# Performance work log

Hardware: AMD Instinct MI355X
Metric: run time of the kernel (lower is better)

## Reference

```python
import jax, jax.numpy as jnp
import numpy as np
from math import factorial

LMAX = 2
C_DIM = 128
N = 50000
# (l1, l2, l_out) 'uuu' (channel-wise, no weights) instructions, as in the module ([:3])
INSTR = [(2, 2, 0), (1, 2, 1), (1, 1, 2)]


def _f(n):
    return float(factorial(int(n)))


def _su2_cg(j1, m1, j2, m2, j3, m3):
    # Clebsch-Gordan <j1 m1 j2 m2 | j3 m3> (Racah formula), complex SU(2) basis
    if m3 != m1 + m2:
        return 0.0
    vmin = int(max(-j1 + j2 + m3, -j1 + m1, 0))
    vmax = int(min(j2 + j3 + m1, j3 - j1 + j2, j3 + m3))
    pref = ((2 * j3 + 1) * _f(j3 + j1 - j2) * _f(j3 - j1 + j2) * _f(j1 + j2 - j3) / _f(j1 + j2 + j3 + 1)
            * _f(j3 + m3) * _f(j3 - m3) / (_f(j1 - m1) * _f(j1 + m1) * _f(j2 - m2) * _f(j2 + m2))) ** 0.5
    s = 0.0
    for v in range(vmin, vmax + 1):
        s += (-1.0) ** (v + j2 + m2) / _f(v) * _f(j2 + j3 + m1 - v) * _f(j1 - m1 + v) / (
            _f(j3 - j1 + j2 - v) * _f(j3 + m3 - v) * _f(v + j1 - j2 - m3))
    return pref * s


def _q_real_to_complex(l):
    # e3nn change-of-basis from real to complex spherical harmonics
    q = np.zeros((2 * l + 1, 2 * l + 1), dtype=np.complex128)
    for m in range(-l, 0):
        q[l + m, l + abs(m)] = 1.0 / np.sqrt(2)
        q[l + m, l - abs(m)] = -1j / np.sqrt(2)
    q[l, l] = 1.0
    for m in range(1, l + 1):
        q[l + m, l + abs(m)] = (-1) ** m / np.sqrt(2)
        q[l + m, l - abs(m)] = 1j * (-1) ** m / np.sqrt(2)
    return (-1j) ** l * q


def wigner_3j(l1, l2, l3):
    # real-basis Wigner 3j, unit Frobenius norm (e3nn convention)
    Csu2 = np.zeros((2 * l1 + 1, 2 * l2 + 1, 2 * l3 + 1), dtype=np.complex128)
    for i, m1 in enumerate(range(-l1, l1 + 1)):
        for k, m2 in enumerate(range(-l2, l2 + 1)):
            for n, m3 in enumerate(range(-l3, l3 + 1)):
                Csu2[i, k, n] = _su2_cg(l1, m1, l2, m2, l3, m3)
    Q1, Q2, Q3 = _q_real_to_complex(l1), _q_real_to_complex(l2), _q_real_to_complex(l3)
    C = np.einsum('ij,kl,mn,ikn->jlm', Q1, Q2, np.conj(Q3.T), Csu2)
    assert np.abs(C.imag).max() < 1e-7
    C = C.real
    return (C / np.linalg.norm(C)).astype(np.float32)


W3J = {(l1, l2, lo): jnp.asarray(wigner_3j(l1, l2, lo)) for (l1, l2, lo) in INSTR}


def so3_linear(x, W, b):
    # per-degree block-diagonal linear; x: [N, (LMAX+1)^2, Cin], W: [LMAX+1, Cout, Cin], b: [Cout] (l=0 only)
    outs = []
    for l in range(LMAX + 1):
        y = jnp.einsum('nmc,dc->nmd', x[:, l * l:(l + 1) * (l + 1), :], W[l])
        if l == 0:
            y = y + b
        outs.append(y)
    return jnp.concatenate(outs, axis=1)


def tensor_product_uuu(x1, x2):
    # sparse CG tensor product, channel-shared ('uuu'), no path weights
    out = jnp.zeros_like(x1)
    for (l1, l2, lo) in INSTR:
        w3j = W3J[(l1, l2, lo)]
        alpha = float((2 * lo + 1) ** 0.5)  # component normalization
        blk = alpha * jnp.einsum('ijk,nic,njc->nkc', w3j,
                                 x1[:, l1 * l1:(l1 + 1) ** 2, :],
                                 x2[:, l2 * l2:(l2 + 1) ** 2, :])
        out = out.at[:, lo * lo:(lo + 1) ** 2, :].add(blk)
    return out


def setup_inputs() -> dict:
    key = jax.random.key(0)
    ks = jax.random.split(key, 7)
    scale = 1.0 / np.sqrt(C_DIM)
    m_dim = (LMAX + 1) ** 2  # 9
    return {
        'irreps_x': jax.random.normal(ks[0], (N, m_dim, C_DIM), jnp.float32),
        'W_left': jax.random.normal(ks[1], (LMAX + 1, C_DIM, C_DIM), jnp.float32) * scale,
        'b_left': jax.random.normal(ks[2], (C_DIM,), jnp.float32) * scale,
        'W_right': jax.random.normal(ks[3], (LMAX + 1, C_DIM, C_DIM), jnp.float32) * scale,
        'b_right': jax.random.normal(ks[4], (C_DIM,), jnp.float32) * scale,
        'W_final': jax.random.normal(ks[5], (LMAX + 1, C_DIM, C_DIM), jnp.float32) * scale,
        'b_final': jax.random.normal(ks[6], (C_DIM,), jnp.float32) * scale,
    }


def reference(irreps_x, W_left, b_left, W_right, b_right, W_final, b_final):
    xl = so3_linear(irreps_x, W_left, b_left)
    xr = so3_linear(irreps_x, W_right, b_right)
    out = tensor_product_uuu(xl, xr)
    return so3_linear(out, W_final, b_final)  # [N, 9, C]
```

## Files before the change

### kernel.cpp

```cpp
#include <hip/hip_runtime.h>
#include <cmath>
#include <complex>

typedef unsigned short u16;
typedef __bf16 bf16x8 __attribute__((ext_vector_type(8)));
typedef float f32x4 __attribute__((ext_vector_type(4)));

#define CD 128
#define TILE_N 8
#define XS 136
#define LS 128

#define SMEM_TOTAL (72 * XS + 64 * LS + 64 * LS)

struct TPW { float w220[25]; float w121[45]; float w112[45]; };

__device__ __forceinline__ u16 f2b(float f) {
  unsigned u = __float_as_uint(f);
  u += 0x7fffu + ((u >> 16) & 1u);
  return (u16)(u >> 16);
}
__device__ __forceinline__ float b2f(u16 h) {
  return __uint_as_float(((unsigned)h) << 16);
}

__global__ void cvt_weights_kernel(const float* __restrict__ Wl,
                                   const float* __restrict__ Wr,
                                   const float* __restrict__ Wf,
                                   u16* __restrict__ ws) {
  int idx = blockIdx.x * 256 + threadIdx.x;
  const float* src; int off;
  if (idx < 49152)      { src = Wl; off = idx; }
  else if (idx < 98304) { src = Wr; off = idx - 49152; }
  else                  { src = Wf; off = idx - 98304; }
  ws[idx] = f2b(src[off]);
}

__global__ __launch_bounds__(256, 3)
void fused_kernel(const float* __restrict__ x, const u16* __restrict__ ws,
                  const float* __restrict__ bfin, float* __restrict__ out,
                  int N, TPW tw) {
  __shared__ __align__(16) u16 smem[SMEM_TOTAL];
  u16* bufX = smem;
  u16* sTP  = smem;
  u16* sL   = smem + 72 * XS;
  u16* sR   = smem + 72 * XS + 64 * LS;

  const int tid  = threadIdx.x;
  const int n0   = blockIdx.x * TILE_N;
  const int w    = tid >> 6;
  const int lane = tid & 63;
  const int q    = lane >> 4;
  const int lr   = lane & 15;

#pragma unroll
  for (int it = 0; it < 4; ++it) {
    int e = (it * 256 + tid) * 8;
    int r = e >> 7;
    int c = e & 127;
    int n = n0 + (r & 7);
    if (n >= N) n = N - 1;
    int grow = (n * 9 + 1 + (r >> 3)) * CD + c;
    float4 a = *(const float4*)(x + grow);
    float4 b = *(const float4*)(x + grow + 4);
    uint4 v;
    v.x = (unsigned)f2b(a.x) | ((unsigned)f2b(a.y) << 16);
    v.y = (unsigned)f2b(a.z) | ((unsigned)f2b(a.w) << 16);
    v.z = (unsigned)f2b(b.x) | ((unsigned)f2b(b.y) << 16);
    v.w = (unsigned)f2b(b.z) | ((unsigned)f2b(b.w) << 16);
    *(uint4*)(bufX + r * XS + c) = v;
  }
  __syncthreads();

#pragma unroll
  for (int cti = 0; cti < 4; ++cti) {
    int ct   = w * 4 + cti;
    int mat  = ct >> 3;
    int dcol = ((ct & 7) << 4) + lr;
    const u16* w1 = ws + (mat * 3 + 1) * 16384 + dcol * CD;
    const u16* w2 = ws + (mat * 3 + 2) * 16384 + dcol * CD;
    uint4 b1[4], b2[4];
#pragma unroll
    for (int kk = 0; kk < 4; ++kk) {
      b1[kk] = *(const uint4*)(w1 + kk * 32 + q * 8);
      b2[kk] = *(const uint4*)(w2 + kk * 32 + q * 8);
    }
    u16* dst = (ct < 8) ? sL : sR;
#pragma unroll
    for (int rt = 0; rt < 5; ++rt) {
      const int l2f   = (rt >= 2) ? 1 : 0;
      const int rows  = l2f ? 40 : 24;
      const int gbase = l2f ? (rt - 2) * 16 : rt * 16;
      const int boff  = l2f ? 24 : 0;
      int ga = gbase + lr; if (ga > rows - 1) ga = rows - 1;
      const int arow = boff + ga;
      f32x4 acc = {0.f, 0.f, 0.f, 0.f};
#pragma unroll
      for (int kk = 0; kk < 4; ++kk) {
        uint4 av = *(const uint4*)(bufX + arow * XS + kk * 32 + q * 8);
        acc = __builtin_amdgcn_mfma_f32_16x16x32_bf16(
            __builtin_bit_cast(bf16x8, av),
            __builtin_bit_cast(bf16x8, l2f ? b2[kk] : b1[kk]),
            acc, 0, 0, 0);
      }
#pragma unroll
      for (int reg = 0; reg < 4; ++reg) {
        int gg = gbase + q * 4 + reg;
        if (gg < rows) dst[(boff + gg) * LS + dcol] = f2b(acc[reg]);
      }
    }
  }
  __syncthreads();

  {
    int c  = tid & 127;
    int nb = tid >> 7;
#pragma unroll
    for (int p = 0; p < 4; ++p) {
      int n = nb * 4 + p;
      float xl1[3], xr1[3], xl2[5], xr2[5];
#pragma unroll
      for (int i = 0; i < 3; ++i) {
        xl1[i] = b2f(sL[(i * 8 + n) * LS + c]);
        xr1[i] = b2f(sR[(i * 8 + n) * LS + c]);
      }
#pragma unroll
      for (int j = 0; j < 5; ++j) {
        xl2[j] = b2f(sL[(24 + j * 8 + n) * LS + c]);
        xr2[j] = b2f(sR[(24 + j * 8 + n) * LS + c]);
      }
      float o0 = 0.f;
#pragma unroll
      for (int i = 0; i < 5; ++i)
#pragma unroll
        for (int j = 0; j < 5; ++j)
          o0 += tw.w220[i * 5 + j] * xl2[i] * xr2[j];
      float o1[3] = {0.f, 0.f, 0.f};
#pragma unroll
      for (int i = 0; i < 3; ++i)
#pragma unroll
        for (int j = 0; j < 5; ++j) {
          float pr = xl1[i] * xr2[j];
#pragma unroll
          for (int k = 0; k < 3; ++k) o1[k] += tw.w121[(i * 5 + j) * 3 + k] * pr;
        }
      float o2[5] = {0.f, 0.f, 0.f, 0.f, 0.f};
#pragma unroll
      for (int i = 0; i < 3; ++i)
#pragma unroll
        for (int j = 0; j < 3; ++j) {
          float pr = xl1[i] * xr1[j];
#pragma unroll
          for (int k = 0; k < 5; ++k) o2[k] += tw.w112[(i * 3 + j) * 5 + k] * pr;
        }
      sTP[(0 * 8 + n) * XS + c] = f2b(o0);
#pragma unroll
      for (int k = 0; k < 3; ++k) sTP[((1 + k) * 8 + n) * XS + c] = f2b(o1[k]);
#pragma unroll
      for (int k = 0; k < 5; ++k) sTP[((4 + k) * 8 + n) * XS + c] = f2b(o2[k]);
    }
  }
  __syncthreads();

#pragma unroll
  for (int cti = 0; cti < 2; ++cti) {
    int ct   = w + cti * 4;
    int dcol = (ct << 4) + lr;
    float bias = bfin[dcol];
    const u16* wfb = ws + 6 * 16384 + dcol * CD;
#pragma unroll
    for (int l = 0; l < 3; ++l) {
      const u16* wf = wfb + l * 16384;
      uint4 bfrag[4];
#pragma unroll
      for (int kk = 0; kk < 4; ++kk)
        bfrag[kk] = *(const uint4*)(wf + kk * 32 + q * 8);
      const int rows   = (l == 0) ? 8 : (l == 1 ? 24 : 40);
      const int soff   = (l == 0) ? 0 : (l == 1 ? 8 : 32);
      const int ntiles = (l == 0) ? 1 : (l == 1 ? 2 : 3);
      for (int t = 0; t < ntiles; ++t) {
        int ga = t * 16 + lr; if (ga > rows - 1) ga = rows - 1;
        const int arow = soff + ga;
        f32x4 acc = {0.f, 0.f, 0.f, 0.f};
#pragma unroll
        for (int kk = 0; kk < 4; ++kk) {
          uint4 av = *(const uint4*)(sTP + arow * XS + kk * 32 + q * 8);
          acc = __builtin_amdgcn_mfma_f32_16x16x32_bf16(
              __builtin_bit_cast(bf16x8, av),
              __builtin_bit_cast(bf16x8, bfrag[kk]),
              acc, 0, 0, 0);
        }
#pragma unroll
        for (int reg = 0; reg < 4; ++reg) {
          int gg = t * 16 + q * 4 + reg;
          if (gg < rows) {
            int m = l * l + (gg >> 3);
            int n = n0 + (gg & 7);
            if (n < N) {
              float v = acc[reg];
              if (l == 0) v += bias;
              out[(n * 9 + m) * CD + dcol] = v;
            }
          }
        }
      }
    }
  }
}

typedef std::complex<double> cd;

static double factd(int n) { double r = 1.0; for (int i = 2; i <= n; ++i) r *= i; return r; }

static double su2_cg(int j1, int m1, int j2, int m2, int j3, int m3) {
  if (m3 != m1 + m2) return 0.0;
  int vmin = -j1 + j2 + m3; if (-j1 + m1 > vmin) vmin = -j1 + m1; if (0 > vmin) vmin = 0;
  int vmax = j2 + j3 + m1; if (j3 - j1 + j2 < vmax) vmax = j3 - j1 + j2; if (j3 + m3 < vmax) vmax = j3 + m3;
  double pref = std::sqrt((2.0 * j3 + 1.0) * factd(j3 + j1 - j2) * factd(j3 - j1 + j2)
                          * factd(j1 + j2 - j3) / factd(j1 + j2 + j3 + 1)
                          * factd(j3 + m3) * factd(j3 - m3)
                          / (factd(j1 - m1) * factd(j1 + m1) * factd(j2 - m2) * factd(j2 + m2)));
  double s = 0.0;
  for (int v = vmin; v <= vmax; ++v) {
    double sgn = ((v + j2 + m2) & 1) ? -1.0 : 1.0;
    s += sgn / factd(v) * factd(j2 + j3 + m1 - v) * factd(j1 - m1 + v)
         / (factd(j3 - j1 + j2 - v) * factd(j3 + m3 - v) * factd(v + j1 - j2 - m3));
  }
  return pref * s;
}

static void qmat(int l, cd q[5][5]) {
  for (int a = 0; a < 5; ++a) for (int b = 0; b < 5; ++b) q[a][b] = 0.0;
  const double is2 = 1.0 / std::sqrt(2.0);
  for (int m = -l; m < 0; ++m) {
    q[l + m][l - m] = is2;
    q[l + m][l + m] = cd(0.0, -is2);
  }
  q[l][l] = 1.0;
  for (int m = 1; m <= l; ++m) {
    double s = (m & 1) ? -1.0 : 1.0;
    q[l + m][l + m] = s * is2;
    q[l + m][l - m] = cd(0.0, s * is2);
  }
  cd f(1.0, 0.0);
  for (int i = 0; i < l; ++i) f *= cd(0.0, -1.0);
  for (int a = 0; a < 5; ++a) for (int b = 0; b < 5; ++b) q[a][b] *= f;
}

static void wigner3j(int l1, int l2, int l3, double* C) {
  int d1 = 2 * l1 + 1, d2 = 2 * l2 + 1, d3 = 2 * l3 + 1;
  cd Q1[5][5], Q2[5][5], Q3[5][5];
  qmat(l1, Q1); qmat(l2, Q2); qmat(l3, Q3);
  cd Csu2[5][5][5];
  for (int i = 0; i < d1; ++i)
    for (int k = 0; k < d2; ++k)
      for (int n = 0; n < d3; ++n)
        Csu2[i][k][n] = su2_cg(l1, i - l1, l2, k - l2, l3, n - l3);
  double norm = 0.0;
  for (int j = 0; j < d1; ++j)
    for (int lx = 0; lx < d2; ++lx)
      for (int m = 0; m < d3; ++m) {
        cd acc(0.0, 0.0);
        for (int i = 0; i < d1; ++i)
          for (int k = 0; k < d2; ++k)
            for (int n = 0; n < d3; ++n)
              acc += Q1[i][j] * Q2[k][lx] * std::conj(Q3[n][m]) * Csu2[i][k][n];
        C[(j * d2 + lx) * d3 + m] = acc.real();
        norm += acc.real() * acc.real();
      }
  norm = std::sqrt(norm);
  for (int t = 0; t < d1 * d2 * d3; ++t) C[t] /= norm;
}

extern "C" void kernel_launch(void* const* d_in, const int* in_sizes, int n_in,
                              void* d_out, int out_size, void* d_ws, size_t ws_size,
                              hipStream_t stream) {
  const float* x    = (const float*)d_in[0];
  const float* Wl   = (const float*)d_in[1];
  const float* Wr   = (const float*)d_in[3];
  const float* Wf   = (const float*)d_in[5];
  const float* bfin = (const float*)d_in[6];
  float* out = (float*)d_out;
  const int N = in_sizes[0] / (9 * CD);

  TPW tw;
  double c220[25], c121[45], c112[45];
  wigner3j(2, 2, 0, c220);
  wigner3j(1, 2, 1, c121);
  wigner3j(1, 1, 2, c112);
  const double a1 = std::sqrt(3.0), a2 = std::sqrt(5.0);
  for (int i = 0; i < 25; ++i) tw.w220[i] = (float)c220[i];
  for (int i = 0; i < 45; ++i) tw.w121[i] = (float)(a1 * c121[i]);
  for (int i = 0; i < 45; ++i) tw.w112[i] = (float)(a2 * c112[i]);

  u16* ws = (u16*)d_ws;
  cvt_weights_kernel<<<576, 256, 0, stream>>>(Wl, Wr, Wf, ws);
  int grid = (N + TILE_N - 1) / TILE_N;
  fused_kernel<<<grid, 256, 0, stream>>>(x, ws, bfin, out, N, tw);
}
```

Baseline: 522.5 us.

## Restructure fused kernel: prefetch weight fragments, reuse A tiles, vectorize TP stage

Weight B-fragments for the left/right linears and the bias are loaded before the x tile is staged, so their global latency overlaps the input conversion. Each wave now owns one matrix and reuses loaded A fragments across two column tiles. The final linear computes two column tiles per A load and prefetches its weights before the barrier. The tensor-product stage handles two channels per thread with 32-bit LDS accesses, and the LDS row stride is padded to 132. The weight-conversion kernel is vectorized to 8 elements per thread. Holding more fragments in flight raises register pressure, which may hurt occupancy under the launch bounds of 3 blocks.

```diff
diff --git a/kernel.cpp b/kernel.cpp
--- a/kernel.cpp
+++ b/kernel.cpp
@@ -3,13 +3,14 @@
 #include <complex>
 
 typedef unsigned short u16;
+typedef unsigned int u32;
 typedef __bf16 bf16x8 __attribute__((ext_vector_type(8)));
 typedef float f32x4 __attribute__((ext_vector_type(4)));
 
 #define CD 128
 #define TILE_N 8
 #define XS 136
-#define LS 128
+#define LS 132
 
 #define SMEM_TOTAL (72 * XS + 64 * LS + 64 * LS)
 
@@ -23,17 +24,27 @@
 __device__ __forceinline__ float b2f(u16 h) {
   return __uint_as_float(((unsigned)h) << 16);
 }
+__device__ __forceinline__ u32 pack2(float a, float b) {
+  return (u32)f2b(a) | ((u32)f2b(b) << 16);
+}
 
 __global__ void cvt_weights_kernel(const float* __restrict__ Wl,
                                    const float* __restrict__ Wr,
                                    const float* __restrict__ Wf,
                                    u16* __restrict__ ws) {
-  int idx = blockIdx.x * 256 + threadIdx.x;
+  int idx = (blockIdx.x * 256 + threadIdx.x) * 8;
   const float* src; int off;
   if (idx < 49152)      { src = Wl; off = idx; }
   else if (idx < 98304) { src = Wr; off = idx - 49152; }
   else                  { src = Wf; off = idx - 98304; }
-  ws[idx] = f2b(src[off]);
+  float4 a = *(const float4*)(src + off);
+  float4 b = *(const float4*)(src + off + 4);
+  uint4 v;
+  v.x = pack2(a.x, a.y);
+  v.y = pack2(a.z, a.w);
+  v.z = pack2(b.x, b.y);
+  v.w = pack2(b.z, b.w);
+  *(uint4*)(ws + idx) = v;
 }
 
 __global__ __launch_bounds__(256, 3)
@@ -52,6 +63,26 @@
   const int lane = tid & 63;
   const int q    = lane >> 4;
   const int lr   = lane & 15;
+
+  const int mat = w >> 1;
+  const int wl  = w & 1;
+  u16* dstA = mat ? sR : sL;
+  const u16* wsA = ws + mat * 3 * 16384;
+
+  uint4 bfa[2][2][4];
+#pragma unroll
+  for (int ci = 0; ci < 2; ++ci) {
+    int dcol = (wl * 4 + ci) * 16 + lr;
+#pragma unroll
+    for (int kk = 0; kk < 4; ++kk) {
+      bfa[ci][0][kk] = *(const uint4*)(wsA + 16384     + dcol * CD + kk * 32 + q * 8);
+      bfa[ci][1][kk] = *(const uint4*)(wsA + 2 * 16384 + dcol * CD + kk * 32 + q * 8);
+    }
+  }
+  const int dc0 = w * 16 + lr;
+  const int dc1 = dc0 + 64;
+  float bias0 = bfin[dc0];
+  float bias1 = bfin[dc1];
 
 #pragma unroll
   for (int it = 0; it < 4; ++it) {
@@ -64,28 +95,27 @@
     float4 a = *(const float4*)(x + grow);
     float4 b = *(const float4*)(x + grow + 4);
     uint4 v;
-    v.x = (unsigned)f2b(a.x) | ((unsigned)f2b(a.y) << 16);
-    v.y = (unsigned)f2b(a.z) | ((unsigned)f2b(a.w) << 16);
-    v.z = (unsigned)f2b(b.x) | ((unsigned)f2b(b.y) << 16);
-    v.w = (unsigned)f2b(b.z) | ((unsigned)f2b(b.w) << 16);
+    v.x = pack2(a.x, a.y);
+    v.y = pack2(a.z, a.w);
+    v.z = pack2(b.x, b.y);
+    v.w = pack2(b.z, b.w);
     *(uint4*)(bufX + r * XS + c) = v;
   }
   __syncthreads();
 
 #pragma unroll
-  for (int cti = 0; cti < 4; ++cti) {
-    int ct   = w * 4 + cti;
-    int mat  = ct >> 3;
-    int dcol = ((ct & 7) << 4) + lr;
-    const u16* w1 = ws + (mat * 3 + 1) * 16384 + dcol * CD;
-    const u16* w2 = ws + (mat * 3 + 2) * 16384 + dcol * CD;
-    uint4 b1[4], b2[4];
-#pragma unroll
-    for (int kk = 0; kk < 4; ++kk) {
-      b1[kk] = *(const uint4*)(w1 + kk * 32 + q * 8);
-      b2[kk] = *(const uint4*)(w2 + kk * 32 + q * 8);
-    }
-    u16* dst = (ct < 8) ? sL : sR;
+  for (int p = 0; p < 2; ++p) {
+    if (p == 1) {
+#pragma unroll
+      for (int ci = 0; ci < 2; ++ci) {
+        int dcol = (wl * 4 + 2 + ci) * 16 + lr;
+#pragma unroll
+        for (int kk = 0; kk < 4; ++kk) {
+          bfa[ci][0][kk] = *(const uint4*)(wsA + 16384     + dcol * CD + kk * 32 + q * 8);
+          bfa[ci][1][kk] = *(const uint4*)(wsA + 2 * 16384 + dcol * CD + kk * 32 + q * 8);
+        }
+      }
+    }
 #pragma unroll
     for (int rt = 0; rt < 5; ++rt) {
       const int l2f   = (rt >= 2) ? 1 : 0;
@@ -94,113 +124,146 @@
       const int boff  = l2f ? 24 : 0;
       int ga = gbase + lr; if (ga > rows - 1) ga = rows - 1;
       const int arow = boff + ga;
-      f32x4 acc = {0.f, 0.f, 0.f, 0.f};
+      uint4 av[4];
+#pragma unroll
+      for (int kk = 0; kk < 4; ++kk)
+        av[kk] = *(const uint4*)(bufX + arow * XS + kk * 32 + q * 8);
+#pragma unroll
+      for (int ci = 0; ci < 2; ++ci) {
+        int dcol = (wl * 4 + 2 * p + ci) * 16 + lr;
+        f32x4 acc = {0.f, 0.f, 0.f, 0.f};
+#pragma unroll
+        for (int kk = 0; kk < 4; ++kk) {
+          acc = __builtin_amdgcn_mfma_f32_16x16x32_bf16(
+              __builtin_bit_cast(bf16x8, av[kk]),
+              __builtin_bit_cast(bf16x8, bfa[ci][l2f][kk]),
+              acc, 0, 0, 0);
+        }
+#pragma unroll
+        for (int reg = 0; reg < 4; ++reg) {
+          int gg = gbase + q * 4 + reg;
+          if (gg < rows) dstA[(boff + gg) * LS + dcol] = f2b(acc[reg]);
+        }
+      }
+    }
+  }
+  __syncthreads();
+
+#pragma unroll
+  for (int iter = 0; iter < 2; ++iter) {
+    int id = iter * 256 + tid;
+    int cb = (id & 63) * 2;
+    int n  = id >> 6;
+    const u16* pL = sL + n * LS + cb;
+    const u16* pR = sR + n * LS + cb;
+    float xl1[2][3], xr1[2][3], xl2[2][5], xr2[2][5];
+#pragma unroll
+    for (int i = 0; i < 3; ++i) {
+      u32 vl = *(const u32*)(pL + i * 8 * LS);
+      u32 vr = *(const u32*)(pR + i * 8 * LS);
+      xl1[0][i] = b2f((u16)vl); xl1[1][i] = b2f((u16)(vl >> 16));
+      xr1[0][i] = b2f((u16)vr); xr1[1][i] = b2f((u16)(vr >> 16));
+    }
+#pragma unroll
+    for (int j = 0; j < 5; ++j) {
+      u32 vl = *(const u32*)(pL + (24 + j * 8) * LS);
+      u32 vr = *(const u32*)(pR + (24 + j * 8) * LS);
+      xl2[0][j] = b2f((u16)vl); xl2[1][j] = b2f((u16)(vl >> 16));
+      xr2[0][j] = b2f((u16)vr); xr2[1][j] = b2f((u16)(vr >> 16));
+    }
+    float o0[2], o1[2][3], o2[2][5];
+#pragma unroll
+    for (int ch = 0; ch < 2; ++ch) {
+      float s0 = 0.f;
+#pragma unroll
+      for (int i = 0; i < 5; ++i)
+#pragma unroll
+        for (int j = 0; j < 5; ++j)
+          s0 += tw.w220[i * 5 + j] * xl2[ch][i] * xr2[ch][j];
+      o0[ch] = s0;
+      float a1[3] = {0.f, 0.f, 0.f};
+#pragma unroll
+      for (int i = 0; i < 3; ++i)
+#pragma unroll
+        for (int j = 0; j < 5; ++j) {
+          float pr = xl1[ch][i] * xr2[ch][j];
+#pragma unroll
+          for (int k = 0; k < 3; ++k) a1[k] += tw.w121[(i * 5 + j) * 3 + k] * pr;
+        }
+#pragma unroll
+      for (int k = 0; k < 3; ++k) o1[ch][k] = a1[k];
+      float a2[5] = {0.f, 0.f, 0.f, 0.f, 0.f};
+#pragma unroll
+      for (int i = 0; i < 3; ++i)
+#pragma unroll
+        for (int j = 0; j < 3; ++j) {
+          float pr = xl1[ch][i] * xr1[ch][j];
+#pragma unroll
+          for (int k = 0; k < 5; ++k) a2[k] += tw.w112[(i * 3 + j) * 5 + k] * pr;
+        }
+#pragma unroll
+      for (int k = 0; k < 5; ++k) o2[ch][k] = a2[k];
+    }
+    u16* pT = sTP + n * XS + cb;
+    *(u32*)(pT) = pack2(o0[0], o0[1]);
+#pragma unroll
+    for (int k = 0; k < 3; ++k) *(u32*)(pT + (1 + k) * 8 * XS) = pack2(o1[0][k], o1[1][k]);
+#pragma unroll
+    for (int k = 0; k < 5; ++k) *(u32*)(pT + (4 + k) * 8 * XS) = pack2(o2[0][k], o2[1][k]);
+  }
+
+  const u16* wsf = ws + 6 * 16384;
+  uint4 bc0[4], bc1[4];
+#pragma unroll
+  for (int kk = 0; kk < 4; ++kk) {
+    bc0[kk] = *(const uint4*)(wsf + dc0 * CD + kk * 32 + q * 8);
+    bc1[kk] = *(const uint4*)(wsf + dc1 * CD + kk * 32 + q * 8);
+  }
+  __syncthreads();
+
+#pragma unroll
+  for (int l = 0; l < 3; ++l) {
+    if (l > 0) {
 #pragma unroll
       for (int kk = 0; kk < 4; ++kk) {
-        uint4 av = *(const uint4*)(bufX + arow * XS + kk * 32 + q * 8);
-        acc = __builtin_amdgcn_mfma_f32_16x16x32_bf16(
-            __builtin_bit_cast(bf16x8, av),
-            __builtin_bit_cast(bf16x8, l2f ? b2[kk] : b1[kk]),
-            acc, 0, 0, 0);
+        bc0[kk] = *(const uint4*)(wsf + l * 16384 + dc0 * CD + kk * 32 + q * 8);
+        bc1[kk] = *(const uint4*)(wsf + l * 16384 + dc1 * CD + kk * 32 + q * 8);
+      }
+    }
+    const int rows   = (l == 0) ? 8 : (l == 1 ? 24 : 40);
+    const int soff   = (l == 0) ? 0 : (l == 1 ? 8 : 32);
+    const int ntiles = (l == 0) ? 1 : (l == 1 ? 2 : 3);
+#pragma unroll
+    for (int t = 0; t < 3; ++t) {
+      if (t >= ntiles) continue;
+      int ga = t * 16 + lr; if (ga > rows - 1) ga = rows - 1;
+      const int arow = soff + ga;
+      uint4 av[4];
+#pragma unroll
+      for (int kk = 0; kk < 4; ++kk)
+        av[kk] = *(const uint4*)(sTP + arow * XS + kk * 32 + q * 8);
+      f32x4 a0 = {0.f, 0.f, 0.f, 0.f};
+      f32x4 a1 = {0.f, 0.f, 0.f, 0.f};
+#pragma unroll
+      for (int kk = 0; kk < 4; ++kk) {
+        a0 = __builtin_amdgcn_mfma_f32_16x16x32_bf16(
+            __builtin_bit_cast(bf16x8, av[kk]),
+            __builtin_bit_cast(bf16x8, bc0[kk]), a0, 0, 0, 0);
+        a1 = __builtin_amdgcn_mfma_f32_16x16x32_bf16(
+            __builtin_bit_cast(bf16x8, av[kk]),
+            __builtin_bit_cast(bf16x8, bc1[kk]), a1, 0, 0, 0);
       }
 #pragma unroll
       for (int reg = 0; reg < 4; ++reg) {
-        int gg = gbase + q * 4 + reg;
-        if (gg < rows) dst[(boff + gg) * LS + dcol] = f2b(acc[reg]);
-      }
-    }
-  }
-  __syncthreads();
-
-  {
-    int c  = tid & 127;
-    int nb = tid >> 7;
-#pragma unroll
-    for (int p = 0; p < 4; ++p) {
-      int n = nb * 4 + p;
-      float xl1[3], xr1[3], xl2[5], xr2[5];
-#pragma unroll
-      for (int i = 0; i < 3; ++i) {
-        xl1[i] = b2f(sL[(i * 8 + n) * LS + c]);
-        xr1[i] = b2f(sR[(i * 8 + n) * LS + c]);
-      }
-#pragma unroll
-      for (int j = 0; j < 5; ++j) {
-        xl2[j] = b2f(sL[(24 + j * 8 + n) * LS + c]);
-        xr2[j] = b2f(sR[(24 + j * 8 + n) * LS + c]);
-      }
-      float o0 = 0.f;
-#pragma unroll
-      for (int i = 0; i < 5; ++i)
-#pragma unroll
-        for (int j = 0; j < 5; ++j)
-          o0 += tw.w220[i * 5 + j] * xl2[i] * xr2[j];
-      float o1[3] = {0.f, 0.f, 0.f};
-#pragma unroll
-      for (int i = 0; i < 3; ++i)
-#pragma unroll
-        for (int j = 0; j < 5; ++j) {
-          float pr = xl1[i] * xr2[j];
-#pragma unroll
-          for (int k = 0; k < 3; ++k) o1[k] += tw.w121[(i * 5 + j) * 3 + k] * pr;
-        }
-      float o2[5] = {0.f, 0.f, 0.f, 0.f, 0.f};
-#pragma unroll
-      for (int i = 0; i < 3; ++i)
-#pragma unroll
-        for (int j = 0; j < 3; ++j) {
-          float pr = xl1[i] * xr1[j];
-#pragma unroll
-          for (int k = 0; k < 5; ++k) o2[k] += tw.w112[(i * 3 + j) * 5 + k] * pr;
-        }
-      sTP[(0 * 8 + n) * XS + c] = f2b(o0);
-#pragma unroll
-      for (int k = 0; k < 3; ++k) sTP[((1 + k) * 8 + n) * XS + c] = f2b(o1[k]);
-#pragma unroll
-      for (int k = 0; k < 5; ++k) sTP[((4 + k) * 8 + n) * XS + c] = f2b(o2[k]);
-    }
-  }
-  __syncthreads();
-
-#pragma unroll
-  for (int cti = 0; cti < 2; ++cti) {
-    int ct   = w + cti * 4;
-    int dcol = (ct << 4) + lr;
-    float bias = bfin[dcol];
-    const u16* wfb = ws + 6 * 16384 + dcol * CD;
-#pragma unroll
-    for (int l = 0; l < 3; ++l) {
-      const u16* wf = wfb + l * 16384;
-      uint4 bfrag[4];
-#pragma unroll
-      for (int kk = 0; kk < 4; ++kk)
-        bfrag[kk] = *(const uint4*)(wf + kk * 32 + q * 8);
-      const int rows   = (l == 0) ? 8 : (l == 1 ? 24 : 40);
-      const int soff   = (l == 0) ? 0 : (l == 1 ? 8 : 32);
-      const int ntiles = (l == 0) ? 1 : (l == 1 ? 2 : 3);
-      for (int t = 0; t < ntiles; ++t) {
-        int ga = t * 16 + lr; if (ga > rows - 1) ga = rows - 1;
-        const int arow = soff + ga;
-        f32x4 acc = {0.f, 0.f, 0.f, 0.f};
-#pragma unroll
-        for (int kk = 0; kk < 4; ++kk) {
-          uint4 av = *(const uint4*)(sTP + arow * XS + kk * 32 + q * 8);
-          acc = __builtin_amdgcn_mfma_f32_16x16x32_bf16(
-              __builtin_bit_cast(bf16x8, av),
-              __builtin_bit_cast(bf16x8, bfrag[kk]),
-              acc, 0, 0, 0);
-        }
-#pragma unroll
-        for (int reg = 0; reg < 4; ++reg) {
-          int gg = t * 16 + q * 4 + reg;
-          if (gg < rows) {
-            int m = l * l + (gg >> 3);
-            int n = n0 + (gg & 7);
-            if (n < N) {
-              float v = acc[reg];
-              if (l == 0) v += bias;
-              out[(n * 9 + m) * CD + dcol] = v;
-            }
+        int gg = t * 16 + q * 4 + reg;
+        if (gg < rows) {
+          int m = l * l + (gg >> 3);
+          int n = n0 + (gg & 7);
+          if (n < N) {
+            float v0 = a0[reg], v1 = a1[reg];
+            if (l == 0) { v0 += bias0; v1 += bias1; }
+            out[(n * 9 + m) * CD + dc0] = v0;
+            out[(n * 9 + m) * CD + dc1] = v1;
           }
         }
       }
@@ -294,7 +357,7 @@
   for (int i = 0; i < 45; ++i) tw.w112[i] = (float)(a2 * c112[i]);
 
   u16* ws = (u16*)d_ws;
-  cvt_weights_kernel<<<576, 256, 0, stream>>>(Wl, Wr, Wf, ws);
+  cvt_weights_kernel<<<72, 256, 0, stream>>>(Wl, Wr, Wf, ws);
   int grid = (N + TILE_N - 1) / TILE_N;
   fused_kernel<<<grid, 256, 0, stream>>>(x, ws, bfin, out, N, tw);
 }
```

Result: faster. 503.4 us (-3.6%).
